# Performance work log

Measured on AMD Instinct MI355X. Metric: run time of the kernel, lower is better.

The kernel has to match this reference:

```python
import jax, jax.numpy as jnp
import numpy as np
import math

FEAT, HID, EMB, NCLS = 128, 128, 64, 10
N, E = 50000, 1600000
RATIO = 0.8


def graph_conv(x, src, dst, valid, w_rel, b_rel, w_root):
    # PyG GraphConv: out = lin_rel(sum_{j->i} x_j) + lin_root(x_i)
    msg = jnp.where(valid[:, None], x[src], 0.0)  # [E, C]
    seg = jnp.where(valid, dst, x.shape[0])       # invalid -> dummy bucket
    agg = jax.ops.segment_sum(msg, seg, num_segments=x.shape[0] + 1)[:-1]
    return agg @ w_rel.T + b_rel + x @ w_root.T


def topk_pool(x, src, dst, valid, weight):
    # PyG TopKPooling: score = tanh((x . w) / ||w||); keep top ceil(ratio*N)
    score = jnp.tanh((x @ weight) / jnp.linalg.norm(weight))
    k = int(math.ceil(RATIO * x.shape[0]))
    _, perm = jax.lax.top_k(score, k)
    xp = x[perm] * score[perm][:, None]
    mapping = jnp.full((x.shape[0],), -1, dtype=src.dtype)
    mapping = mapping.at[perm].set(jnp.arange(k, dtype=src.dtype))
    nsrc, ndst = mapping[src], mapping[dst]
    nvalid = valid & (nsrc >= 0) & (ndst >= 0)
    return xp, nsrc, ndst, nvalid, perm


def setup_inputs() -> dict:
    key = jax.random.key(0)
    ks = jax.random.split(key, 24)
    s = 0.05
    inp = {
        'x': jax.random.normal(ks[0], (N, FEAT), dtype=jnp.float32),
        'edge_index': jax.random.randint(ks[1], (2, E), 0, N, dtype=jnp.int32),
        'w1_rel': jax.random.normal(ks[2], (HID, FEAT)) * s,
        'w1_root': jax.random.normal(ks[3], (HID, FEAT)) * s,
        'b1': jnp.zeros((HID,), jnp.float32),
        'p1_w': jax.random.normal(ks[4], (HID,)) * s,
        'w2_rel': jax.random.normal(ks[5], (EMB, HID)) * s,
        'w2_root': jax.random.normal(ks[6], (EMB, HID)) * s,
        'b2': jnp.zeros((EMB,), jnp.float32),
        'p2_w': jax.random.normal(ks[7], (EMB,)) * s,
        'w3_rel': jax.random.normal(ks[8], (EMB, EMB)) * s,
        'w3_root': jax.random.normal(ks[9], (EMB, EMB)) * s,
        'b3': jnp.zeros((EMB,), jnp.float32),
        'w4_rel': jax.random.normal(ks[10], (HID, EMB)) * s,
        'w4_root': jax.random.normal(ks[11], (HID, EMB)) * s,
        'b4': jnp.zeros((HID,), jnp.float32),
        'w5_rel': jax.random.normal(ks[12], (FEAT, HID)) * s,
        'w5_root': jax.random.normal(ks[13], (FEAT, HID)) * s,
        'b5': jnp.zeros((FEAT,), jnp.float32),
        'lin_w': jax.random.normal(ks[14], (NCLS, FEAT)) * s,
        'lin_b': jnp.zeros((NCLS,), jnp.float32),
    }
    return inp


def reference(x, edge_index, w1_rel, w1_root, b1, p1_w, w2_rel, w2_root, b2, p2_w,
              w3_rel, w3_root, b3, w4_rel, w4_root, b4, w5_rel, w5_root, b5,
              lin_w, lin_b):
    src0, dst0 = edge_index[0], edge_index[1]
    valid0 = jnp.ones((src0.shape[0],), dtype=bool)

    x1 = jax.nn.relu(graph_conv(x, src0, dst0, valid0, w1_rel, b1, w1_root))
    xp1, src1, dst1, valid1, perm1 = topk_pool(x1, src0, dst0, valid0, p1_w)
    x2 = jax.nn.relu(graph_conv(xp1, src1, dst1, valid1, w2_rel, b2, w2_root))
    xp2, src2, dst2, valid2, perm2 = topk_pool(x2, src1, dst1, valid1, p2_w)
    x3 = jax.nn.relu(graph_conv(xp2, src2, dst2, valid2, w3_rel, b3, w3_root))
    # Unpool1: scatter x3 into zeros shaped like x2, then skip-add
    u1 = jnp.zeros((x2.shape[0], x3.shape[1]), x3.dtype).at[perm2].set(x3) + x2
    x4 = jax.nn.relu(graph_conv(u1, src1, dst1, valid1, w4_rel, b4, w4_root))
    # Unpool2
    u2 = jnp.zeros((x1.shape[0], x4.shape[1]), x4.dtype).at[perm1].set(x4) + x1
    x5 = jax.nn.relu(graph_conv(u2, src0, dst0, valid0, w5_rel, b5, w5_root))
    return jax.nn.log_softmax(x5 @ lin_w.T + lin_b, axis=-1)
```

## Files before the change

kernel.cpp:

```cpp
#include <hip/hip_runtime.h>
#include <hip/hip_bf16.h>
#include <math.h>

#define N0 50000
#define E0 1600000
#define K1 40000
#define K2 32000
#define FEAT 128
#define HID 128
#define EMB 64
#define NCLS 10

#define RADIX_BINS 4096

#define NB 391
#define PB_CH 8192
#define BCAP 5120

#define SCHUNK 2048

typedef __bf16 v8bf __attribute__((ext_vector_type(8)));
typedef __bf16 v4bf __attribute__((ext_vector_type(4)));
typedef float  v4f  __attribute__((ext_vector_type(4)));
typedef unsigned short u16;

static __device__ __forceinline__ unsigned f2key(float f) {
    unsigned u = __float_as_uint(f);
    return (u & 0x80000000u) ? ~u : (u | 0x80000000u);
}

__global__ void detect_dtype_kernel(const unsigned* __restrict__ w, int n, int* __restrict__ flag) {
    __shared__ int tot;
    if (threadIdx.x == 0) tot = 0;
    __syncthreads();
    int cnt = 0;
    for (int i = threadIdx.x; i < n; i += 256) {
        unsigned lo = w[i] & 0xFFFFu;
        unsigned e = (lo >> 7) & 0xFFu;
        cnt += (e >= 143);
    }
    atomicAdd(&tot, cnt);
    __syncthreads();
    if (threadIdx.x == 0) flag[0] = (tot > n / 8) ? 1 : 0;
}

static __device__ __forceinline__ float load_as_f32(const void* in, long long i, int isF32) {
    if (isF32) return ((const float*)in)[i];
    unsigned short h = ((const unsigned short*)in)[i];
    return __uint_as_float(((unsigned)h) << 16);
}

__global__ void x_convert_kernel(const void* __restrict__ in, float* __restrict__ xf,
                                 __bf16* __restrict__ hi, __bf16* __restrict__ lo, int n,
                                 const int* __restrict__ flag) {
    int i = blockIdx.x * 256 + threadIdx.x;
    if (i >= n) return;
    float v = load_as_f32(in, i, *flag);
    __bf16 h = (__bf16)v;
    int row = i >> 7, c = i & 127;
    xf[(((size_t)(c >> 4)) * N0 + row) * 16 + (c & 15)] = v;
    hi[i] = h; lo[i] = (__bf16)(v - (float)h);
}

struct SplitJob { const void* src; __bf16* hi; __bf16* lo; int n; };
struct SplitJobs { SplitJob j[10]; };
__global__ void split_all_kernel(SplitJobs jobs, const int* __restrict__ flag) {
    SplitJob jb = jobs.j[blockIdx.y];
    int i = blockIdx.x * 256 + threadIdx.x;
    if (i >= jb.n) return;
    float v = load_as_f32(jb.src, i, *flag);
    __bf16 h = (__bf16)v;
    jb.hi[i] = h; jb.lo[i] = (__bf16)(v - (float)h);
}

struct F32Job { const void* src; float* dst; int n; };
struct F32Jobs { F32Job j[9]; };
__global__ void f32_all_kernel(F32Jobs jobs, const int* __restrict__ flag) {
    F32Job jb = jobs.j[blockIdx.x];
    for (int i = threadIdx.x; i < jb.n; i += 256) jb.dst[i] = load_as_f32(jb.src, i, *flag);
}

__global__ void deg_count_kernel(const int* __restrict__ dst, int E, int* __restrict__ deg) {
    int e = blockIdx.x * 256 + threadIdx.x;
    if (e >= E) return;
    atomicAdd(&deg[dst[e]], 1);
}

__global__ void scan_reduce_kernel(const int* __restrict__ deg, int M, int* __restrict__ btot) {
    int t = threadIdx.x;
    int idx = blockIdx.x * SCHUNK + t * 8;
    int s = 0;
    if (idx + 8 <= M) {
        int4 a = *(const int4*)(deg + idx);
        int4 b = *(const int4*)(deg + idx + 4);
        s = a.x + a.y + a.z + a.w + b.x + b.y + b.z + b.w;
    } else {
        for (int k = 0; k < 8; ++k) if (idx + k < M) s += deg[idx + k];
    }
    for (int off = 32; off >= 1; off >>= 1) s += __shfl_xor(s, off, 64);
    __shared__ int ws[4];
    if ((t & 63) == 0) ws[t >> 6] = s;
    __syncthreads();
    if (t == 0) btot[blockIdx.x] = ws[0] + ws[1] + ws[2] + ws[3];
}

__global__ void scan_offsets_kernel(const int* __restrict__ btot, int nb,
                                    int* __restrict__ boff, int* __restrict__ totPtr) {
    int t = threadIdx.x;
    int v = (t < nb) ? btot[t] : 0;
    int incl = v;
    for (int off = 1; off < 64; off <<= 1) {
        int u = __shfl_up(incl, off, 64);
        if (t >= off) incl += u;
    }
    if (t < nb) boff[t] = incl - v;
    if (t == 63 && totPtr) totPtr[0] = incl;
}

__global__ void scan_apply_kernel(const int* __restrict__ deg, int M, const int* __restrict__ boff,
                                  int* __restrict__ rowptr, int* __restrict__ cursor) {
    int t = threadIdx.x;
    int lane = t & 63, wave = t >> 6;
    int idx = blockIdx.x * SCHUNK + t * 8;
    int v[8];
#pragma unroll
    for (int k = 0; k < 8; ++k) v[k] = (idx + k < M) ? deg[idx + k] : 0;
    int s = 0;
#pragma unroll
    for (int k = 0; k < 8; ++k) { int tmp = v[k]; v[k] = s; s += tmp; }
    int incl = s;
    for (int off = 1; off < 64; off <<= 1) {
        int u = __shfl_up(incl, off, 64);
        if (lane >= off) incl += u;
    }
    int texcl = incl - s;
    __shared__ int ws[4];
    if (lane == 63) ws[wave] = incl;
    __syncthreads();
    int woff = 0;
    for (int w = 0; w < 4; ++w) if (w < wave) woff += ws[w];
    int off0 = boff[blockIdx.x] + woff + texcl;
#pragma unroll
    for (int k = 0; k < 8; ++k) {
        int j = idx + k;
        if (j < M) {
            int val = off0 + v[k];
            rowptr[j] = val;
            if (cursor) cursor[j] = val;
        }
    }
}

__global__ void bcur_init_kernel(const int* __restrict__ rp, int* __restrict__ bcur) {
    int b = blockIdx.x * 256 + threadIdx.x;
    if (b < NB) bcur[b] = rp[b << 7];
}

__global__ void edge_partition_kernel(const int* __restrict__ src, const int* __restrict__ dst, int E,
                                      int* __restrict__ bcur, unsigned* __restrict__ pairBuf) {
    __shared__ int cnt[NB];
    __shared__ int bas[NB];
    for (int b = threadIdx.x; b < NB; b += 256) cnt[b] = 0;
    __syncthreads();
    int e0 = blockIdx.x * PB_CH;
    int e1 = E < e0 + PB_CH ? E : e0 + PB_CH;
    for (int e = e0 + threadIdx.x; e < e1; e += 256)
        atomicAdd(&cnt[dst[e] >> 7], 1);
    __syncthreads();
    for (int b = threadIdx.x; b < NB; b += 256) {
        int c = cnt[b];
        bas[b] = c ? atomicAdd(&bcur[b], c) : 0;
        cnt[b] = 0;
    }
    __syncthreads();
    for (int e = e0 + threadIdx.x; e < e1; e += 256) {
        int s = src[e];
        int d = dst[e];
        int b = d >> 7;
        int r = atomicAdd(&cnt[b], 1);
        unsigned pv = ((unsigned)(d & 127) << 16) | (unsigned)s;
        __builtin_nontemporal_store(pv, pairBuf + bas[b] + r);
    }
}

__global__ void bucket_csr_fill_kernel(const unsigned* __restrict__ pairBuf, const int* __restrict__ rp,
                                       int Mrows, u16* __restrict__ cols, int* __restrict__ gcursor) {
    int b = blockIdx.x;
    int d0 = b << 7;
    int d1 = d0 + 128; if (d1 > Mrows) d1 = Mrows;
    int segBase = rp[d0], segEnd = rp[d1];
    int size = segEnd - segBase;
    __shared__ int cur[128];
    __shared__ u16 stage[BCAP];
    if (size <= BCAP) {
        for (int j = threadIdx.x; j < d1 - d0; j += 256) cur[j] = rp[d0 + j] - segBase;
        __syncthreads();
        for (int t = threadIdx.x; t < size; t += 256) {
            unsigned p = pairBuf[segBase + t];
            int pos = atomicAdd(&cur[p >> 16], 1);
            stage[pos] = (u16)(p & 0xFFFFu);
        }
        __syncthreads();
        for (int t = threadIdx.x; t < size; t += 256)
            __builtin_nontemporal_store(stage[t], cols + segBase + t);
    } else {
        for (int t = threadIdx.x; t < size; t += 256) {
            unsigned p = pairBuf[segBase + t];
            int pos = atomicAdd(&gcursor[d0 + (int)(p >> 16)], 1);
            cols[pos] = (u16)(p & 0xFFFFu);
        }
    }
}

__global__ void deg_filter_kernel(const int* __restrict__ rowptr, const u16* __restrict__ cols,
                                  const int* __restrict__ map, int Mold, int* __restrict__ deg) {
    int d = blockIdx.x * 256 + threadIdx.x;
    if (d >= Mold) return;
    int nd = map[d];
    if (nd < 0) return;
    int b = rowptr[d], e = rowptr[d + 1];
    int c = 0;
    for (int j = b; j < e; ++j) c += (map[cols[j]] >= 0);
    deg[nd] = c;
}

__global__ void csr_filter_fill_kernel(const int* __restrict__ rowptr, const u16* __restrict__ cols,
                                       const int* __restrict__ map, int Mold,
                                       const int* __restrict__ newrp, u16* __restrict__ ncols) {
    int d = blockIdx.x * 256 + threadIdx.x;
    if (d >= Mold) return;
    int nd = map[d];
    if (nd < 0) return;
    int w = newrp[nd];
    int b = rowptr[d], e = rowptr[d + 1];
    for (int j = b; j < e; ++j) {
        int ns = map[cols[j]];
        if (ns >= 0) ncols[w++] = (u16)ns;
    }
}

template<int C>
__global__ void __launch_bounds__(256, 8)
aggregate_kernel(const int* __restrict__ rowptr, const u16* __restrict__ cols,
                 const float* __restrict__ xs, __bf16* __restrict__ aggHi,
                 __bf16* __restrict__ aggLo, int M) {
    const int SW = C / 8;
    const int LPR = SW / 4;
    const int RPB = 256 / LPR;
    int sl = blockIdx.x & 7;
    int n  = (blockIdx.x >> 3) * RPB + threadIdx.x / LPR;
    int c4 = threadIdx.x % LPR;
    if (n >= M) return;
    const float* xsl = xs + (size_t)sl * M * SW + (size_t)c4 * 4;
    int b = rowptr[n], e = rowptr[n + 1];
    float4 s = {0.f, 0.f, 0.f, 0.f};
    int j = b;
    for (; j + 8 <= e; j += 8) {
        int i0 = cols[j],     i1 = cols[j + 1], i2 = cols[j + 2], i3 = cols[j + 3];
        int i4 = cols[j + 4], i5 = cols[j + 5], i6 = cols[j + 6], i7 = cols[j + 7];
        float4 v0 = *(const float4*)(xsl + (size_t)i0 * SW);
        float4 v1 = *(const float4*)(xsl + (size_t)i1 * SW);
        float4 v2 = *(const float4*)(xsl + (size_t)i2 * SW);
        float4 v3 = *(const float4*)(xsl + (size_t)i3 * SW);
        float4 v4 = *(const float4*)(xsl + (size_t)i4 * SW);
        float4 v5 = *(const float4*)(xsl + (size_t)i5 * SW);
        float4 v6 = *(const float4*)(xsl + (size_t)i6 * SW);
        float4 v7 = *(const float4*)(xsl + (size_t)i7 * SW);
        s.x += v0.x; s.y += v0.y; s.z += v0.z; s.w += v0.w;
        s.x += v1.x; s.y += v1.y; s.z += v1.z; s.w += v1.w;
        s.x += v2.x; s.y += v2.y; s.z += v2.z; s.w += v2.w;
        s.x += v3.x; s.y += v3.y; s.z += v3.z; s.w += v3.w;
        s.x += v4.x; s.y += v4.y; s.z += v4.z; s.w += v4.w;
        s.x += v5.x; s.y += v5.y; s.z += v5.z; s.w += v5.w;
        s.x += v6.x; s.y += v6.y; s.z += v6.z; s.w += v6.w;
        s.x += v7.x; s.y += v7.y; s.z += v7.z; s.w += v7.w;
    }
    for (; j < e; ++j) {
        int i0 = cols[j];
        float4 v0 = *(const float4*)(xsl + (size_t)i0 * SW);
        s.x += v0.x; s.y += v0.y; s.z += v0.z; s.w += v0.w;
    }
    v4bf h, l;
    h[0] = (__bf16)s.x; l[0] = (__bf16)(s.x - (float)h[0]);
    h[1] = (__bf16)s.y; l[1] = (__bf16)(s.y - (float)h[1]);
    h[2] = (__bf16)s.z; l[2] = (__bf16)(s.z - (float)h[2]);
    h[3] = (__bf16)s.w; l[3] = (__bf16)(s.w - (float)h[3]);
    size_t o = ((size_t)sl * M + n) * SW + c4 * 4;
    __builtin_nontemporal_store(h, (v4bf*)(aggHi + o));
    __builtin_nontemporal_store(l, (v4bf*)(aggLo + o));
}

template<int Cin, int Cout>
__global__ void linear_mfma_kernel(int M,
                                   const __bf16* __restrict__ Ahi, const __bf16* __restrict__ Alo,
                                   const __bf16* __restrict__ WaHi, const __bf16* __restrict__ WaLo,
                                   const __bf16* __restrict__ Bhi, const __bf16* __restrict__ Blo,
                                   const __bf16* __restrict__ WbHi, const __bf16* __restrict__ WbLo,
                                   const float* __restrict__ bias, float* __restrict__ outF) {
    constexpr int NG = Cout / 16;
    constexpr int SW = Cin / 8;
    int wave = threadIdx.x >> 6;
    int lane = threadIdx.x & 63;
    int m = lane & 15, quad = lane >> 4;
    int row0 = blockIdx.x * 64 + wave * 16;
    int ra = row0 + m; if (ra > M - 1) ra = M - 1;

    v4f acc[NG];
#pragma unroll
    for (int g = 0; g < NG; ++g) acc[g] = (v4f){0.f, 0.f, 0.f, 0.f};

#pragma unroll
    for (int ks = 0; ks < Cin / 32; ++ks) {
        int col0 = ks * 32 + quad * 8;
        int sl = col0 / SW, off = col0 % SW;
        size_t aoff = ((size_t)sl * M + ra) * SW + off;
        v8bf ah = *(const v8bf*)(Ahi + aoff);
        v8bf al = *(const v8bf*)(Alo + aoff);
#pragma unroll
        for (int g = 0; g < NG; ++g) {
            size_t woff = (size_t)(g * 16 + m) * Cin + ks * 32 + quad * 8;
            v8bf bh = *(const v8bf*)(WaHi + woff);
            v8bf bl = *(const v8bf*)(WaLo + woff);
            acc[g] = __builtin_amdgcn_mfma_f32_16x16x32_bf16(ah, bh, acc[g], 0, 0, 0);
            acc[g] = __builtin_amdgcn_mfma_f32_16x16x32_bf16(ah, bl, acc[g], 0, 0, 0);
            acc[g] = __builtin_amdgcn_mfma_f32_16x16x32_bf16(al, bh, acc[g], 0, 0, 0);
        }
    }
#pragma unroll
    for (int ks = 0; ks < Cin / 32; ++ks) {
        size_t aoff = (size_t)ra * Cin + ks * 32 + quad * 8;
        v8bf ah = *(const v8bf*)(Bhi + aoff);
        v8bf al = *(const v8bf*)(Blo + aoff);
#pragma unroll
        for (int g = 0; g < NG; ++g) {
            size_t woff = (size_t)(g * 16 + m) * Cin + ks * 32 + quad * 8;
            v8bf bh = *(const v8bf*)(WbHi + woff);
            v8bf bl = *(const v8bf*)(WbLo + woff);
            acc[g] = __builtin_amdgcn_mfma_f32_16x16x32_bf16(ah, bh, acc[g], 0, 0, 0);
            acc[g] = __builtin_amdgcn_mfma_f32_16x16x32_bf16(ah, bl, acc[g], 0, 0, 0);
            acc[g] = __builtin_amdgcn_mfma_f32_16x16x32_bf16(al, bh, acc[g], 0, 0, 0);
        }
    }

#pragma unroll
    for (int g = 0; g < NG; ++g) {
        int col = g * 16 + m;
        float bv = bias[col];
#pragma unroll
        for (int r = 0; r < 4; ++r) {
            int row = row0 + quad * 4 + r;
            if (row < M) outF[(size_t)row * Cout + col] = fmaxf(acc[g][r] + bv, 0.f);
        }
    }
}

template<int C>
__global__ void score_kernel(const float* __restrict__ xin, const float* __restrict__ w,
                             int M, float* __restrict__ score, unsigned long long* __restrict__ keys) {
    int row = blockIdx.x * 4 + (threadIdx.x >> 6);
    int lane = threadIdx.x & 63;
    if (row >= M) return;
    float p = 0.f, q = 0.f;
#pragma unroll
    for (int c = lane; c < C; c += 64) {
        float wc = w[c];
        float xc = xin[(size_t)row * C + c];
        p += xc * wc; q += wc * wc;
    }
#pragma unroll
    for (int off = 32; off >= 1; off >>= 1) {
        p += __shfl_xor(p, off, 64);
        q += __shfl_xor(q, off, 64);
    }
    if (lane == 0) {
        float arg = p / sqrtf(q);
        float sc = (float)tanh((double)arg);
        score[row] = sc;
        keys[row] = ((unsigned long long)f2key(sc) << 16) |
                    (unsigned long long)(0xFFFFu ^ (unsigned)row);
    }
}

struct SelCtl { unsigned long long prefix; int kRem; int counter; };

__global__ void radix_hist_kernel(const unsigned long long* __restrict__ keys, int N,
                                  int* __restrict__ hist, const SelCtl* __restrict__ ctl, int pass) {
    __shared__ int lh[RADIX_BINS];
    for (int b = threadIdx.x; b < RADIX_BINS; b += 256) lh[b] = 0;
    __syncthreads();
    int shift = 36 - 12 * pass;
    unsigned long long pref = (pass > 0) ? ctl->prefix : 0ull;
    for (int i = blockIdx.x * 256 + threadIdx.x; i < N; i += gridDim.x * 256) {
        unsigned long long key = keys[i];
        if (pass > 0 && (key >> (shift + 12)) != pref) continue;
        atomicAdd(&lh[(int)((key >> shift) & 0xFFFull)], 1);
    }
    __syncthreads();
    for (int b = threadIdx.x; b < RADIX_BINS; b += 256) {
        int c = lh[b];
        if (c) atomicAdd(&hist[b], c);
    }
}

__global__ void radix_select_kernel(int* __restrict__ hist, SelCtl* __restrict__ ctl,
                                    int K, int pass) {
    __shared__ int part[1024];
    int t = threadIdx.x;
    int kRem = (pass == 0) ? K : ctl->kRem;
    unsigned long long oldPrefix = (pass == 0) ? 0ull : ctl->prefix;
    int base = t * 4;
    int h0 = hist[base], h1 = hist[base + 1], h2 = hist[base + 2], h3 = hist[base + 3];
    int tot = h0 + h1 + h2 + h3;
    part[t] = tot;
    __syncthreads();
    for (int off = 1; off < 1024; off <<= 1) {
        int v = (t + off < 1024) ? part[t + off] : 0;
        __syncthreads();
        part[t] += v;
        __syncthreads();
    }
    int sExcl = part[t] - tot;
    if (sExcl < kRem && kRem <= sExcl + tot) {
        int c = sExcl;
        int hv[4] = {h0, h1, h2, h3};
        for (int k = 3; k >= 0; --k) {
            int h = hv[k];
            if (c + h >= kRem) {
                ctl->prefix = (oldPrefix << 12) | (unsigned long long)(base + k);
                ctl->kRem = kRem - c;
                ctl->counter = 0;
                break;
            }
            c += h;
        }
    }
    hist[base] = 0; hist[base + 1] = 0; hist[base + 2] = 0; hist[base + 3] = 0;
}

__global__ void mark_keep_kernel(const unsigned long long* __restrict__ keys, int N,
                                 const SelCtl* __restrict__ ctl, int* __restrict__ keep) {
    int i = blockIdx.x * 256 + threadIdx.x;
    if (i < N) keep[i] = (keys[i] >= ctl->prefix) ? 1 : 0;
}

__global__ void finalize_map_kernel(const int* __restrict__ keep, const int* __restrict__ pos,
                                    int N, int* __restrict__ perm, int* __restrict__ mapping) {
    int i = blockIdx.x * 256 + threadIdx.x;
    if (i >= N) return;
    if (keep[i]) { int r = pos[i]; perm[r] = i; mapping[i] = r; }
    else mapping[i] = -1;
}

template<int C>
__global__ void pool_apply_kernel(const float* __restrict__ xin, const float* __restrict__ score,
                                  const int* __restrict__ perm, float* __restrict__ xpF,
                                  __bf16* __restrict__ xpHi, __bf16* __restrict__ xpLo, int K) {
    const int CH = C / 4;
    const int SW = C / 8;
    int tid = blockIdx.x * 256 + threadIdx.x;
    int j = tid / CH, c4 = tid % CH;
    if (j >= K) return;
    int src = perm[j];
    float s = score[src];
    float4 v = ((const float4*)(xin + (size_t)src * C))[c4];
    v.x *= s; v.y *= s; v.z *= s; v.w *= s;
    int sl = (c4 * 4) / SW, off = (c4 * 4) % SW;
    *(float4*)(xpF + ((size_t)sl * K + j) * SW + off) = v;
    v4bf h, l;
    h[0] = (__bf16)v.x; l[0] = (__bf16)(v.x - (float)h[0]);
    h[1] = (__bf16)v.y; l[1] = (__bf16)(v.y - (float)h[1]);
    h[2] = (__bf16)v.z; l[2] = (__bf16)(v.z - (float)h[2]);
    h[3] = (__bf16)v.w; l[3] = (__bf16)(v.w - (float)h[3]);
    *(v4bf*)(xpHi + (size_t)j * C + c4 * 4) = h;
    *(v4bf*)(xpLo + (size_t)j * C + c4 * 4) = l;
}

template<int C>
__global__ void unpool_add_kernel(const float* __restrict__ base, const float* __restrict__ deep,
                                  const int* __restrict__ mapping, float* __restrict__ uF,
                                  __bf16* __restrict__ uHi, __bf16* __restrict__ uLo, int M) {
    const int CH = C / 4;
    const int SW = C / 8;
    int tid = blockIdx.x * 256 + threadIdx.x;
    int j = tid / CH, c4 = tid % CH;
    if (j >= M) return;
    float4 v = ((const float4*)(base + (size_t)j * C))[c4];
    int m = mapping[j];
    if (m >= 0) {
        float4 d = ((const float4*)(deep + (size_t)m * C))[c4];
        v.x += d.x; v.y += d.y; v.z += d.z; v.w += d.w;
    }
    int sl = (c4 * 4) / SW, off = (c4 * 4) % SW;
    *(float4*)(uF + ((size_t)sl * M + j) * SW + off) = v;
    v4bf h, l;
    h[0] = (__bf16)v.x; l[0] = (__bf16)(v.x - (float)h[0]);
    h[1] = (__bf16)v.y; l[1] = (__bf16)(v.y - (float)h[1]);
    h[2] = (__bf16)v.z; l[2] = (__bf16)(v.z - (float)h[2]);
    h[3] = (__bf16)v.w; l[3] = (__bf16)(v.w - (float)h[3]);
    *(v4bf*)(uHi + (size_t)j * C + c4 * 4) = h;
    *(v4bf*)(uLo + (size_t)j * C + c4 * 4) = l;
}

__global__ void head_kernel(const float* __restrict__ x5, const float* __restrict__ lw,
                            const float* __restrict__ lb, void* __restrict__ out, int M,
                            const int* __restrict__ flag) {
    int row = blockIdx.x * 4 + (threadIdx.x >> 6);
    int lane = threadIdx.x & 63;
    if (row >= M) return;
    float a0 = x5[(size_t)row * 128 + lane];
    float a1 = x5[(size_t)row * 128 + 64 + lane];
    float d[NCLS];
#pragma unroll
    for (int o = 0; o < NCLS; ++o) {
        float p = a0 * lw[o * 128 + lane] + a1 * lw[o * 128 + 64 + lane];
#pragma unroll
        for (int off = 32; off >= 1; off >>= 1) p += __shfl_xor(p, off, 64);
        d[o] = p + lb[o];
    }
    float mx = d[0];
#pragma unroll
    for (int o = 1; o < NCLS; ++o) mx = fmaxf(mx, d[o]);
    float s = 0.f;
#pragma unroll
    for (int o = 0; o < NCLS; ++o) s += expf(d[o] - mx);
    float lse = mx + logf(s);
    if (lane < NCLS) {
        float v = d[0];
#pragma unroll
        for (int o = 1; o < NCLS; ++o) if (lane == o) v = d[o];
        float r = v - lse;
        if (*flag) ((float*)out)[(size_t)row * NCLS + lane] = r;
        else ((__hip_bfloat16*)out)[(size_t)row * NCLS + lane] = __float2bfloat16(r);
    }
}

extern "C" void kernel_launch(void* const* d_in, const int* in_sizes, int n_in,
                              void* d_out, int out_size, void* d_ws, size_t ws_size,
                              hipStream_t stream) {
    const void* x_raw   = d_in[0];
    const int*  ei      = (const int*)d_in[1];
    const void* w1_rel  = d_in[2];
    const void* w1_root = d_in[3];
    const void* b1      = d_in[4];
    const void* p1w     = d_in[5];
    const void* w2_rel  = d_in[6];
    const void* w2_root = d_in[7];
    const void* b2      = d_in[8];
    const void* p2w     = d_in[9];
    const void* w3_rel  = d_in[10];
    const void* w3_root = d_in[11];
    const void* b3      = d_in[12];
    const void* w4_rel  = d_in[13];
    const void* w4_root = d_in[14];
    const void* b4      = d_in[15];
    const void* w5_rel  = d_in[16];
    const void* w5_root = d_in[17];
    const void* b5      = d_in[18];
    const void* lw      = d_in[19];
    const void* lb      = d_in[20];

    char* base = (char*)d_ws;
    size_t off = 0;
    auto alloc = [&](size_t bytes) -> void* {
        void* p = base + off;
        off = (off + bytes + 255) & ~(size_t)255;
        return p;
    };
    int* flag = (int*)alloc(256);
    __bf16* w1rHi = (__bf16*)alloc(HID * FEAT * 2); __bf16* w1rLo = (__bf16*)alloc(HID * FEAT * 2);
    __bf16* w1tHi = (__bf16*)alloc(HID * FEAT * 2); __bf16* w1tLo = (__bf16*)alloc(HID * FEAT * 2);
    __bf16* w2rHi = (__bf16*)alloc(EMB * HID * 2);  __bf16* w2rLo = (__bf16*)alloc(EMB * HID * 2);
    __bf16* w2tHi = (__bf16*)alloc(EMB * HID * 2);  __bf16* w2tLo = (__bf16*)alloc(EMB * HID * 2);
    __bf16* w3rHi = (__bf16*)alloc(EMB * EMB * 2);  __bf16* w3rLo = (__bf16*)alloc(EMB * EMB * 2);
    __bf16* w3tHi = (__bf16*)alloc(EMB * EMB * 2);  __bf16* w3tLo = (__bf16*)alloc(EMB * EMB * 2);
    __bf16* w4rHi = (__bf16*)alloc(HID * EMB * 2);  __bf16* w4rLo = (__bf16*)alloc(HID * EMB * 2);
    __bf16* w4tHi = (__bf16*)alloc(HID * EMB * 2);  __bf16* w4tLo = (__bf16*)alloc(HID * EMB * 2);
    __bf16* w5rHi = (__bf16*)alloc(FEAT * HID * 2); __bf16* w5rLo = (__bf16*)alloc(FEAT * HID * 2);
    __bf16* w5tHi = (__bf16*)alloc(FEAT * HID * 2); __bf16* w5tLo = (__bf16*)alloc(FEAT * HID * 2);
    float* b1f = (float*)alloc(HID * 4);
    float* b2f = (float*)alloc(EMB * 4);
    float* b3f = (float*)alloc(EMB * 4);
    float* b4f = (float*)alloc(HID * 4);
    float* b5f = (float*)alloc(FEAT * 4);
    float* p1f = (float*)alloc(HID * 4);
    float* p2f = (float*)alloc(EMB * 4);
    float* lwf = (float*)alloc(NCLS * FEAT * 4);
    float* lbf = (float*)alloc(NCLS * 4);
    float* score = (float*)alloc((size_t)N0 * 4);
    unsigned long long* keys = (unsigned long long*)alloc((size_t)N0 * 8);
    int* hist = (int*)alloc((size_t)RADIX_BINS * 4);
    SelCtl* ctl = (SelCtl*)alloc(256);
    int* btot = (int*)alloc(64 * 4);
    int* boff = (int*)alloc(64 * 4);
    int* perm1 = (int*)alloc((size_t)K1 * 4);
    int* map1  = (int*)alloc((size_t)N0 * 4);
    int* perm2 = (int*)alloc((size_t)K2 * 4);
    int* map2  = (int*)alloc((size_t)K1 * 4);
    int* keep  = (int*)alloc((size_t)(N0 + 1) * 4);
    int* pos   = (int*)alloc((size_t)(N0 + 1) * 4);
    int* deg   = (int*)alloc((size_t)(N0 + 1) * 4);
    int* cursor= (int*)alloc((size_t)(N0 + 1) * 4);
    int* rp0   = (int*)alloc((size_t)(N0 + 1) * 4);
    int* rp1   = (int*)alloc((size_t)(K1 + 1) * 4);
    int* rp2   = (int*)alloc((size_t)(K2 + 1) * 4);
    int* bcur  = (int*)alloc((size_t)NB * 4);
    u16* cols0 = (u16*)alloc((size_t)E0 * 2);
    u16* cols1 = (u16*)alloc((size_t)E0 * 2);
    u16* cols2 = (u16*)alloc((size_t)E0 * 2);
    char* ubuf = (char*)alloc((size_t)K1 * 64 * 4 + (size_t)N0 * 128 * 4);
    unsigned* pairBuf = (unsigned*)ubuf;
    float* u1s = (float*)ubuf;
    float* u2s = (float*)(ubuf + (size_t)K1 * 64 * 4);
    char*   arenaX  = (char*)alloc((size_t)N0 * 128 * 4);
    __bf16* arenaHi = (__bf16*)alloc((size_t)N0 * 128 * 2);
    __bf16* arenaLo = (__bf16*)alloc((size_t)N0 * 128 * 2);
    __bf16* aggHi   = (__bf16*)alloc((size_t)N0 * 128 * 2);
    __bf16* aggLo   = (__bf16*)alloc((size_t)N0 * 128 * 2);
    float*  x1f     = (float*)alloc((size_t)N0 * 128 * 4);
    float*  x2f     = (float*)alloc((size_t)K1 * 64 * 4);

    float* xf   = (float*)arenaX;
    float* xp1f = (float*)arenaX;
    float* xp2f = (float*)arenaX;
    float* x3f  = (float*)(arenaX + 8388608);
    float* x4f  = (float*)arenaX;
    float* x5f  = (float*)arenaX;
    __bf16 *xHi = arenaHi,  *xLo = arenaLo;
    __bf16 *xp1Hi = arenaHi, *xp1Lo = arenaLo;
    __bf16 *xp2Hi = arenaHi, *xp2Lo = arenaLo;
    __bf16 *u1Hi = arenaHi,  *u1Lo = arenaLo;
    __bf16 *u2Hi = arenaHi,  *u2Lo = arenaLo;

    const int* src0 = ei;
    const int* dst0 = ei + E0;

    auto g = [](long long n, int b) -> unsigned { return (unsigned)((n + b - 1) / b); };

    auto run_scan = [&](const int* degp, int M, int* rowp, int* curp) {
        int nb = (M + SCHUNK - 1) / SCHUNK;
        scan_reduce_kernel<<<nb, 256, 0, stream>>>(degp, M, btot);
        scan_offsets_kernel<<<1, 64, 0, stream>>>(btot, nb, boff, rowp + M);
        scan_apply_kernel<<<nb, 256, 0, stream>>>(degp, M, boff, rowp, curp);
    };

    detect_dtype_kernel<<<1, 256, 0, stream>>>((const unsigned*)x_raw, 4096, flag);
    hipMemsetAsync(hist, 0, (size_t)RADIX_BINS * 4, stream);
    x_convert_kernel<<<g((long long)N0 * FEAT, 256), 256, 0, stream>>>(x_raw, xf, xHi, xLo, N0 * FEAT, flag);
    {
        SplitJobs sj;
        sj.j[0] = {w1_rel,  w1rHi, w1rLo, HID * FEAT};
        sj.j[1] = {w1_root, w1tHi, w1tLo, HID * FEAT};
        sj.j[2] = {w2_rel,  w2rHi, w2rLo, EMB * HID};
        sj.j[3] = {w2_root, w2tHi, w2tLo, EMB * HID};
        sj.j[4] = {w3_rel,  w3rHi, w3rLo, EMB * EMB};
        sj.j[5] = {w3_root, w3tHi, w3tLo, EMB * EMB};
        sj.j[6] = {w4_rel,  w4rHi, w4rLo, HID * EMB};
        sj.j[7] = {w4_root, w4tHi, w4tLo, HID * EMB};
        sj.j[8] = {w5_rel,  w5rHi, w5rLo, FEAT * HID};
        sj.j[9] = {w5_root, w5tHi, w5tLo, FEAT * HID};
        dim3 grid(g(HID * FEAT, 256), 10);
        split_all_kernel<<<grid, 256, 0, stream>>>(sj, flag);
    }
    {
        F32Jobs fj;
        fj.j[0] = {b1, b1f, HID};
        fj.j[1] = {b2, b2f, EMB};
        fj.j[2] = {b3, b3f, EMB};
        fj.j[3] = {b4, b4f, HID};
        fj.j[4] = {b5, b5f, FEAT};
        fj.j[5] = {p1w, p1f, HID};
        fj.j[6] = {p2w, p2f, EMB};
        fj.j[7] = {lw, lwf, NCLS * FEAT};
        fj.j[8] = {lb, lbf, NCLS};
        f32_all_kernel<<<9, 256, 0, stream>>>(fj, flag);
    }

    hipMemsetAsync(deg, 0, (size_t)N0 * 4, stream);
    deg_count_kernel<<<g(E0, 256), 256, 0, stream>>>(dst0, E0, deg);
    run_scan(deg, N0, rp0, cursor);
    bcur_init_kernel<<<2, 256, 0, stream>>>(rp0, bcur);
    edge_partition_kernel<<<g(E0, PB_CH), 256, 0, stream>>>(src0, dst0, E0, bcur, pairBuf);
    bucket_csr_fill_kernel<<<NB, 256, 0, stream>>>(pairBuf, rp0, N0, cols0, cursor);

    aggregate_kernel<128><<<g(N0, 64) * 8, 256, 0, stream>>>(rp0, cols0, xf, aggHi, aggLo, N0);
    linear_mfma_kernel<128, 128><<<g(N0, 64), 256, 0, stream>>>(N0, aggHi, aggLo, w1rHi, w1rLo,
                                                                xHi, xLo, w1tHi, w1tLo, b1f, x1f);

    score_kernel<128><<<g(N0, 4), 256, 0, stream>>>(x1f, p1f, N0, score, keys);
    for (int pass = 0; pass < 4; ++pass) {
        radix_hist_kernel<<<64, 256, 0, stream>>>(keys, N0, hist, ctl, pass);
        radix_select_kernel<<<1, 1024, 0, stream>>>(hist, ctl, K1, pass);
    }
    mark_keep_kernel<<<g(N0, 256), 256, 0, stream>>>(keys, N0, ctl, keep);
    run_scan(keep, N0, pos, nullptr);
    finalize_map_kernel<<<g(N0, 256), 256, 0, stream>>>(keep, pos, N0, perm1, map1);
    pool_apply_kernel<128><<<g((long long)K1 * 32, 256), 256, 0, stream>>>(x1f, score, perm1, xp1f, xp1Hi, xp1Lo, K1);

    deg_filter_kernel<<<g(N0, 256), 256, 0, stream>>>(rp0, cols0, map1, N0, deg);
    run_scan(deg, K1, rp1, nullptr);
    csr_filter_fill_kernel<<<g(N0, 256), 256, 0, stream>>>(rp0, cols0, map1, N0, rp1, cols1);

    aggregate_kernel<128><<<g(K1, 64) * 8, 256, 0, stream>>>(rp1, cols1, xp1f, aggHi, aggLo, K1);
    linear_mfma_kernel<128, 64><<<g(K1, 64), 256, 0, stream>>>(K1, aggHi, aggLo, w2rHi, w2rLo,
                                                               xp1Hi, xp1Lo, w2tHi, w2tLo, b2f, x2f);

    score_kernel<64><<<g(K1, 4), 256, 0, stream>>>(x2f, p2f, K1, score, keys);
    for (int pass = 0; pass < 4; ++pass) {
        radix_hist_kernel<<<64, 256, 0, stream>>>(keys, K1, hist, ctl, pass);
        radix_select_kernel<<<1, 1024, 0, stream>>>(hist, ctl, K2, pass);
    }
    mark_keep_kernel<<<g(K1, 256), 256, 0, stream>>>(keys, K1, ctl, keep);
    run_scan(keep, K1, pos, nullptr);
    finalize_map_kernel<<<g(K1, 256), 256, 0, stream>>>(keep, pos, K1, perm2, map2);
    pool_apply_kernel<64><<<g((long long)K2 * 16, 256), 256, 0, stream>>>(x2f, score, perm2, xp2f, xp2Hi, xp2Lo, K2);

    deg_filter_kernel<<<g(K1, 256), 256, 0, stream>>>(rp1, cols1, map2, K1, deg);
    run_scan(deg, K2, rp2, nullptr);
    csr_filter_fill_kernel<<<g(K1, 256), 256, 0, stream>>>(rp1, cols1, map2, K1, rp2, cols2);

    aggregate_kernel<64><<<g(K2, 128) * 8, 256, 0, stream>>>(rp2, cols2, xp2f, aggHi, aggLo, K2);
    linear_mfma_kernel<64, 64><<<g(K2, 64), 256, 0, stream>>>(K2, aggHi, aggLo, w3rHi, w3rLo,
                                                              xp2Hi, xp2Lo, w3tHi, w3tLo, b3f, x3f);

    unpool_add_kernel<64><<<g((long long)K1 * 16, 256), 256, 0, stream>>>(x2f, x3f, map2, u1s, u1Hi, u1Lo, K1);

    aggregate_kernel<64><<<g(K1, 128) * 8, 256, 0, stream>>>(rp1, cols1, u1s, aggHi, aggLo, K1);
    linear_mfma_kernel<64, 128><<<g(K1, 64), 256, 0, stream>>>(K1, aggHi, aggLo, w4rHi, w4rLo,
                                                               u1Hi, u1Lo, w4tHi, w4tLo, b4f, x4f);

    unpool_add_kernel<128><<<g((long long)N0 * 32, 256), 256, 0, stream>>>(x1f, x4f, map1, u2s, u2Hi, u2Lo, N0);

    aggregate_kernel<128><<<g(N0, 64) * 8, 256, 0, stream>>>(rp0, cols0, u2s, aggHi, aggLo, N0);
    linear_mfma_kernel<128, 128><<<g(N0, 64), 256, 0, stream>>>(N0, aggHi, aggLo, w5rHi, w5rLo,
                                                                u2Hi, u2Lo, w5tHi, w5tLo, b5f, x5f);

    head_kernel<<<g(N0, 4), 256, 0, stream>>>(x5f, lwf, lbf, d_out, N0, flag);
}
```

Measured before the change: 1.018 ms.

## Build CSR from bucket counts and fold keep-mask into key-based scans

Replaces the per-edge global-atomic degree count plus full-length scan with a per-block shared-memory bucket count, a single-block scan over the bucket totals, and per-bucket local row counting that writes rowptr inside the fill kernel. The top-k keep mask is no longer materialised; the scan and finalize kernels compare keys against the selected threshold directly. The radix select's block-wide shared-memory suffix scan becomes a wave-shuffle scan. This removes millions of global atomics, several launches and some intermediate buffers, at the cost of reading pairBuf twice in the fill kernel and re-reading keys in several kernels.

```diff
diff --git a/kernel.cpp b/kernel.cpp
--- a/kernel.cpp
+++ b/kernel.cpp
@@ -80,12 +80,6 @@
     for (int i = threadIdx.x; i < jb.n; i += 256) jb.dst[i] = load_as_f32(jb.src, i, *flag);
 }
 
-__global__ void deg_count_kernel(const int* __restrict__ dst, int E, int* __restrict__ deg) {
-    int e = blockIdx.x * 256 + threadIdx.x;
-    if (e >= E) return;
-    atomicAdd(&deg[dst[e]], 1);
-}
-
 __global__ void scan_reduce_kernel(const int* __restrict__ deg, int M, int* __restrict__ btot) {
     int t = threadIdx.x;
     int idx = blockIdx.x * SCHUNK + t * 8;
@@ -118,7 +112,7 @@
 }
 
 __global__ void scan_apply_kernel(const int* __restrict__ deg, int M, const int* __restrict__ boff,
-                                  int* __restrict__ rowptr, int* __restrict__ cursor) {
+                                  int* __restrict__ rowptr) {
     int t = threadIdx.x;
     int lane = t & 63, wave = t >> 6;
     int idx = blockIdx.x * SCHUNK + t * 8;
@@ -143,17 +137,94 @@
 #pragma unroll
     for (int k = 0; k < 8; ++k) {
         int j = idx + k;
-        if (j < M) {
-            int val = off0 + v[k];
-            rowptr[j] = val;
-            if (cursor) cursor[j] = val;
-        }
-    }
-}
-
-__global__ void bcur_init_kernel(const int* __restrict__ rp, int* __restrict__ bcur) {
-    int b = blockIdx.x * 256 + threadIdx.x;
-    if (b < NB) bcur[b] = rp[b << 7];
+        if (j < M) rowptr[j] = off0 + v[k];
+    }
+}
+
+struct SelCtl { unsigned long long prefix; int kRem; int counter; };
+
+__global__ void scan_reduce_keys_kernel(const unsigned long long* __restrict__ keys, int M,
+                                        const SelCtl* __restrict__ ctl, int* __restrict__ btot) {
+    unsigned long long thr = ctl->prefix;
+    int t = threadIdx.x;
+    int idx = blockIdx.x * SCHUNK + t * 8;
+    int s = 0;
+#pragma unroll
+    for (int k = 0; k < 8; ++k) if (idx + k < M) s += (keys[idx + k] >= thr);
+    for (int off = 32; off >= 1; off >>= 1) s += __shfl_xor(s, off, 64);
+    __shared__ int ws[4];
+    if ((t & 63) == 0) ws[t >> 6] = s;
+    __syncthreads();
+    if (t == 0) btot[blockIdx.x] = ws[0] + ws[1] + ws[2] + ws[3];
+}
+
+__global__ void scan_apply_keys_kernel(const unsigned long long* __restrict__ keys, int M,
+                                       const SelCtl* __restrict__ ctl, const int* __restrict__ boff,
+                                       int* __restrict__ pos) {
+    unsigned long long thr = ctl->prefix;
+    int t = threadIdx.x;
+    int lane = t & 63, wave = t >> 6;
+    int idx = blockIdx.x * SCHUNK + t * 8;
+    int v[8];
+#pragma unroll
+    for (int k = 0; k < 8; ++k) v[k] = (idx + k < M) ? (int)(keys[idx + k] >= thr) : 0;
+    int s = 0;
+#pragma unroll
+    for (int k = 0; k < 8; ++k) { int tmp = v[k]; v[k] = s; s += tmp; }
+    int incl = s;
+    for (int off = 1; off < 64; off <<= 1) {
+        int u = __shfl_up(incl, off, 64);
+        if (lane >= off) incl += u;
+    }
+    int texcl = incl - s;
+    __shared__ int ws[4];
+    if (lane == 63) ws[wave] = incl;
+    __syncthreads();
+    int woff = 0;
+    for (int w = 0; w < 4; ++w) if (w < wave) woff += ws[w];
+    int off0 = boff[blockIdx.x] + woff + texcl;
+#pragma unroll
+    for (int k = 0; k < 8; ++k) {
+        int j = idx + k;
+        if (j < M) pos[j] = off0 + v[k];
+    }
+}
+
+__global__ void bucket_count_kernel(const int* __restrict__ dst, int E, int* __restrict__ bktCnt) {
+    __shared__ int cnt[NB];
+    for (int b = threadIdx.x; b < NB; b += 256) cnt[b] = 0;
+    __syncthreads();
+    int e = blockIdx.x * PB_CH;
+    int e1 = E < e + PB_CH ? E : e + PB_CH;
+    for (int i = e + threadIdx.x; i < e1; i += 256)
+        atomicAdd(&cnt[dst[i] >> 7], 1);
+    __syncthreads();
+    for (int b = threadIdx.x; b < NB; b += 256) {
+        int c = cnt[b];
+        if (c) atomicAdd(&bktCnt[b], c);
+    }
+}
+
+__global__ void scan_nb_kernel(const int* __restrict__ bktCnt, int* __restrict__ bktBase,
+                               int* __restrict__ bcur, int* __restrict__ rpM, int E) {
+    __shared__ int sc[512];
+    int t = threadIdx.x;
+    int v = (t < NB) ? bktCnt[t] : 0;
+    sc[t] = v;
+    __syncthreads();
+    for (int off = 1; off < 512; off <<= 1) {
+        int u = 0;
+        if (t >= off) u = sc[t - off];
+        __syncthreads();
+        if (t >= off) sc[t] += u;
+        __syncthreads();
+    }
+    if (t < NB) {
+        int base = sc[t] - v;
+        bktBase[t] = base;
+        bcur[t] = base;
+    }
+    if (t == 0) { bktBase[NB] = E; rpM[0] = E; }
 }
 
 __global__ void edge_partition_kernel(const int* __restrict__ src, const int* __restrict__ dst, int E,
@@ -183,31 +254,52 @@
     }
 }
 
-__global__ void bucket_csr_fill_kernel(const unsigned* __restrict__ pairBuf, const int* __restrict__ rp,
-                                       int Mrows, u16* __restrict__ cols, int* __restrict__ gcursor) {
+__global__ void bucket_fill_kernel(const unsigned* __restrict__ pairBuf, const int* __restrict__ bktBase,
+                                   int Mrows, u16* __restrict__ cols, int* __restrict__ rowptr) {
     int b = blockIdx.x;
     int d0 = b << 7;
     int d1 = d0 + 128; if (d1 > Mrows) d1 = Mrows;
-    int segBase = rp[d0], segEnd = rp[d1];
+    int segBase = bktBase[b], segEnd = bktBase[b + 1];
     int size = segEnd - segBase;
+    int tid = threadIdx.x;
+    __shared__ int cnt[128];
+    __shared__ int sc[128];
     __shared__ int cur[128];
     __shared__ u16 stage[BCAP];
+    if (tid < 128) cnt[tid] = 0;
+    __syncthreads();
+    for (int t = tid; t < size; t += 256)
+        atomicAdd(&cnt[pairBuf[segBase + t] >> 16], 1);
+    __syncthreads();
+    if (tid < 128) sc[tid] = cnt[tid];
+    __syncthreads();
+    for (int off = 1; off < 128; off <<= 1) {
+        int u = 0;
+        if (tid < 128 && tid >= off) u = sc[tid - off];
+        __syncthreads();
+        if (tid < 128 && tid >= off) sc[tid] += u;
+        __syncthreads();
+    }
+    if (tid < 128) {
+        int excl = sc[tid] - cnt[tid];
+        cur[tid] = excl;
+        if (d0 + tid < d1) rowptr[d0 + tid] = segBase + excl;
+    }
+    __syncthreads();
     if (size <= BCAP) {
-        for (int j = threadIdx.x; j < d1 - d0; j += 256) cur[j] = rp[d0 + j] - segBase;
-        __syncthreads();
-        for (int t = threadIdx.x; t < size; t += 256) {
+        for (int t = tid; t < size; t += 256) {
             unsigned p = pairBuf[segBase + t];
             int pos = atomicAdd(&cur[p >> 16], 1);
             stage[pos] = (u16)(p & 0xFFFFu);
         }
         __syncthreads();
-        for (int t = threadIdx.x; t < size; t += 256)
+        for (int t = tid; t < size; t += 256)
             __builtin_nontemporal_store(stage[t], cols + segBase + t);
     } else {
-        for (int t = threadIdx.x; t < size; t += 256) {
+        for (int t = tid; t < size; t += 256) {
             unsigned p = pairBuf[segBase + t];
-            int pos = atomicAdd(&gcursor[d0 + (int)(p >> 16)], 1);
-            cols[pos] = (u16)(p & 0xFFFFu);
+            int pos = atomicAdd(&cur[p >> 16], 1);
+            cols[segBase + pos] = (u16)(p & 0xFFFFu);
         }
     }
 }
@@ -381,8 +473,6 @@
     }
 }
 
-struct SelCtl { unsigned long long prefix; int kRem; int counter; };
-
 __global__ void radix_hist_kernel(const unsigned long long* __restrict__ keys, int N,
                                   int* __restrict__ hist, const SelCtl* __restrict__ ctl, int pass) {
     __shared__ int lh[RADIX_BINS];
@@ -404,22 +494,26 @@
 
 __global__ void radix_select_kernel(int* __restrict__ hist, SelCtl* __restrict__ ctl,
                                     int K, int pass) {
-    __shared__ int part[1024];
+    __shared__ int wtot[16];
     int t = threadIdx.x;
+    int lane = t & 63, wave = t >> 6;
     int kRem = (pass == 0) ? K : ctl->kRem;
     unsigned long long oldPrefix = (pass == 0) ? 0ull : ctl->prefix;
     int base = t * 4;
     int h0 = hist[base], h1 = hist[base + 1], h2 = hist[base + 2], h3 = hist[base + 3];
     int tot = h0 + h1 + h2 + h3;
-    part[t] = tot;
-    __syncthreads();
-    for (int off = 1; off < 1024; off <<= 1) {
-        int v = (t + off < 1024) ? part[t + off] : 0;
-        __syncthreads();
-        part[t] += v;
-        __syncthreads();
-    }
-    int sExcl = part[t] - tot;
+    int incl = tot;
+#pragma unroll
+    for (int off = 1; off < 64; off <<= 1) {
+        int u = __shfl_down(incl, off, 64);
+        if (lane + off < 64) incl += u;
+    }
+    if (lane == 0) wtot[wave] = incl;
+    __syncthreads();
+    int wsuf = 0;
+#pragma unroll
+    for (int w = 0; w < 16; ++w) if (w > wave) wsuf += wtot[w];
+    int sExcl = wsuf + (incl - tot);
     if (sExcl < kRem && kRem <= sExcl + tot) {
         int c = sExcl;
         int hv[4] = {h0, h1, h2, h3};
@@ -437,17 +531,13 @@
     hist[base] = 0; hist[base + 1] = 0; hist[base + 2] = 0; hist[base + 3] = 0;
 }
 
-__global__ void mark_keep_kernel(const unsigned long long* __restrict__ keys, int N,
-                                 const SelCtl* __restrict__ ctl, int* __restrict__ keep) {
-    int i = blockIdx.x * 256 + threadIdx.x;
-    if (i < N) keep[i] = (keys[i] >= ctl->prefix) ? 1 : 0;
-}
-
-__global__ void finalize_map_kernel(const int* __restrict__ keep, const int* __restrict__ pos,
-                                    int N, int* __restrict__ perm, int* __restrict__ mapping) {
+__global__ void finalize_map_keys_kernel(const unsigned long long* __restrict__ keys,
+                                         const int* __restrict__ pos, int N,
+                                         const SelCtl* __restrict__ ctl,
+                                         int* __restrict__ perm, int* __restrict__ mapping) {
     int i = blockIdx.x * 256 + threadIdx.x;
     if (i >= N) return;
-    if (keep[i]) { int r = pos[i]; perm[r] = i; mapping[i] = r; }
+    if (keys[i] >= ctl->prefix) { int r = pos[i]; perm[r] = i; mapping[i] = r; }
     else mapping[i] = -1;
 }
 
@@ -596,13 +686,13 @@
     int* map1  = (int*)alloc((size_t)N0 * 4);
     int* perm2 = (int*)alloc((size_t)K2 * 4);
     int* map2  = (int*)alloc((size_t)K1 * 4);
-    int* keep  = (int*)alloc((size_t)(N0 + 1) * 4);
     int* pos   = (int*)alloc((size_t)(N0 + 1) * 4);
     int* deg   = (int*)alloc((size_t)(N0 + 1) * 4);
-    int* cursor= (int*)alloc((size_t)(N0 + 1) * 4);
     int* rp0   = (int*)alloc((size_t)(N0 + 1) * 4);
     int* rp1   = (int*)alloc((size_t)(K1 + 1) * 4);
     int* rp2   = (int*)alloc((size_t)(K2 + 1) * 4);
+    int* bktCnt = (int*)alloc((size_t)(NB + 1) * 4);
+    int* bktBase= (int*)alloc((size_t)(NB + 1) * 4);
     int* bcur  = (int*)alloc((size_t)NB * 4);
     u16* cols0 = (u16*)alloc((size_t)E0 * 2);
     u16* cols1 = (u16*)alloc((size_t)E0 * 2);
@@ -636,15 +726,22 @@
 
     auto g = [](long long n, int b) -> unsigned { return (unsigned)((n + b - 1) / b); };
 
-    auto run_scan = [&](const int* degp, int M, int* rowp, int* curp) {
+    auto run_scan = [&](const int* degp, int M, int* rowp) {
         int nb = (M + SCHUNK - 1) / SCHUNK;
         scan_reduce_kernel<<<nb, 256, 0, stream>>>(degp, M, btot);
         scan_offsets_kernel<<<1, 64, 0, stream>>>(btot, nb, boff, rowp + M);
-        scan_apply_kernel<<<nb, 256, 0, stream>>>(degp, M, boff, rowp, curp);
+        scan_apply_kernel<<<nb, 256, 0, stream>>>(degp, M, boff, rowp);
+    };
+    auto run_scan_keys = [&](const unsigned long long* keysP, int M, int* posArr) {
+        int nb = (M + SCHUNK - 1) / SCHUNK;
+        scan_reduce_keys_kernel<<<nb, 256, 0, stream>>>(keysP, M, ctl, btot);
+        scan_offsets_kernel<<<1, 64, 0, stream>>>(btot, nb, boff, posArr + M);
+        scan_apply_keys_kernel<<<nb, 256, 0, stream>>>(keysP, M, ctl, boff, posArr);
     };
 
     detect_dtype_kernel<<<1, 256, 0, stream>>>((const unsigned*)x_raw, 4096, flag);
     hipMemsetAsync(hist, 0, (size_t)RADIX_BINS * 4, stream);
+    hipMemsetAsync(bktCnt, 0, (size_t)(NB + 1) * 4, stream);
     x_convert_kernel<<<g((long long)N0 * FEAT, 256), 256, 0, stream>>>(x_raw, xf, xHi, xLo, N0 * FEAT, flag);
     {
         SplitJobs sj;
@@ -675,12 +772,10 @@
         f32_all_kernel<<<9, 256, 0, stream>>>(fj, flag);
     }
 
-    hipMemsetAsync(deg, 0, (size_t)N0 * 4, stream);
-    deg_count_kernel<<<g(E0, 256), 256, 0, stream>>>(dst0, E0, deg);
-    run_scan(deg, N0, rp0, cursor);
-    bcur_init_kernel<<<2, 256, 0, stream>>>(rp0, bcur);
+    bucket_count_kernel<<<g(E0, PB_CH), 256, 0, stream>>>(dst0, E0, bktCnt);
+    scan_nb_kernel<<<1, 512, 0, stream>>>(bktCnt, bktBase, bcur, rp0 + N0, E0);
     edge_partition_kernel<<<g(E0, PB_CH), 256, 0, stream>>>(src0, dst0, E0, bcur, pairBuf);
-    bucket_csr_fill_kernel<<<NB, 256, 0, stream>>>(pairBuf, rp0, N0, cols0, cursor);
+    bucket_fill_kernel<<<NB, 256, 0, stream>>>(pairBuf, bktBase, N0, cols0, rp0);
 
     aggregate_kernel<128><<<g(N0, 64) * 8, 256, 0, stream>>>(rp0, cols0, xf, aggHi, aggLo, N0);
     linear_mfma_kernel<128, 128><<<g(N0, 64), 256, 0, stream>>>(N0, aggHi, aggLo, w1rHi, w1rLo,
@@ -691,13 +786,12 @@
         radix_hist_kernel<<<64, 256, 0, stream>>>(keys, N0, hist, ctl, pass);
         radix_select_kernel<<<1, 1024, 0, stream>>>(hist, ctl, K1, pass);
     }
-    mark_keep_kernel<<<g(N0, 256), 256, 0, stream>>>(keys, N0, ctl, keep);
-    run_scan(keep, N0, pos, nullptr);
-    finalize_map_kernel<<<g(N0, 256), 256, 0, stream>>>(keep, pos, N0, perm1, map1);
+    run_scan_keys(keys, N0, pos);
+    finalize_map_keys_kernel<<<g(N0, 256), 256, 0, stream>>>(keys, pos, N0, ctl, perm1, map1);
     pool_apply_kernel<128><<<g((long long)K1 * 32, 256), 256, 0, stream>>>(x1f, score, perm1, xp1f, xp1Hi, xp1Lo, K1);
 
     deg_filter_kernel<<<g(N0, 256), 256, 0, stream>>>(rp0, cols0, map1, N0, deg);
-    run_scan(deg, K1, rp1, nullptr);
+    run_scan(deg, K1, rp1);
     csr_filter_fill_kernel<<<g(N0, 256), 256, 0, stream>>>(rp0, cols0, map1, N0, rp1, cols1);
 
     aggregate_kernel<128><<<g(K1, 64) * 8, 256, 0, stream>>>(rp1, cols1, xp1f, aggHi, aggLo, K1);
@@ -709,13 +803,12 @@
         radix_hist_kernel<<<64, 256, 0, stream>>>(keys, K1, hist, ctl, pass);
         radix_select_kernel<<<1, 1024, 0, stream>>>(hist, ctl, K2, pass);
     }
-    mark_keep_kernel<<<g(K1, 256), 256, 0, stream>>>(keys, K1, ctl, keep);
-    run_scan(keep, K1, pos, nullptr);
-    finalize_map_kernel<<<g(K1, 256), 256, 0, stream>>>(keep, pos, K1, perm2, map2);
+    run_scan_keys(keys, K1, pos);
+    finalize_map_keys_kernel<<<g(K1, 256), 256, 0, stream>>>(keys, pos, K1, ctl, perm2, map2);
     pool_apply_kernel<64><<<g((long long)K2 * 16, 256), 256, 0, stream>>>(x2f, score, perm2, xp2f, xp2Hi, xp2Lo, K2);
 
     deg_filter_kernel<<<g(K1, 256), 256, 0, stream>>>(rp1, cols1, map2, K1, deg);
-    run_scan(deg, K2, rp2, nullptr);
+    run_scan(deg, K2, rp2);
     csr_filter_fill_kernel<<<g(K1, 256), 256, 0, stream>>>(rp1, cols1, map2, K1, rp2, cols2);
 
     aggregate_kernel<64><<<g(K2, 128) * 8, 256, 0, stream>>>(rp2, cols2, xp2f, aggHi, aggLo, K2);
```

Result: faster. 939.7 us (-7.7%).
